# Performance work log

Hardware: AMD Instinct MI355X
Metric: run time of the kernel (lower is better)

Reference implementation:

```python
import jax, jax.numpy as jnp
import numpy as np

N = 100000
E = 1600000
IN_C, HID_C, OUT_C = 128, 64, 16


def setup_inputs() -> dict:
    key = jax.random.key(0)
    k1, k2, k3, k4, k5 = jax.random.split(key, 5)
    x = jax.random.normal(k1, (N, IN_C), dtype=jnp.float32)
    edge_index = jax.random.randint(k2, (2, E), 0, N, dtype=jnp.int64)
    edge_weight = jax.random.uniform(k3, (E,), dtype=jnp.float32)
    # GCNConv weights (Glorot init, bias=False)
    W1 = jax.random.normal(k4, (IN_C, HID_C), dtype=jnp.float32) * (1.0 / np.sqrt(IN_C))
    W2 = jax.random.normal(k5, (HID_C, OUT_C), dtype=jnp.float32) * (1.0 / np.sqrt(HID_C))
    return {"x": x, "edge_index": edge_index, "edge_weight": edge_weight, "W1": W1, "W2": W2}


def _gcn_norm(edge_index, edge_weight, num_nodes):
    # add self loops with weight 1 (PyG gcn_norm with add_self_loops=True)
    loop = jnp.arange(num_nodes, dtype=edge_index.dtype)
    row = jnp.concatenate([edge_index[0], loop])
    col = jnpp_concat = jnp.concatenate([edge_index[1], loop])
    w = jnp.concatenate([edge_weight, jnp.ones((num_nodes,), edge_weight.dtype)])
    deg = jax.ops.segment_sum(w, col, num_segments=num_nodes)
    dinv = jnp.where(deg > 0, jax.lax.rsqrt(deg), 0.0)
    norm = dinv[row] * w * dinv[col]
    return row, col, norm


def _gcn_conv(x, W, row, col, norm, num_nodes):
    h = x @ W                              # [N, C_out] dense projection
    msg = h[row] * norm[:, None]           # gather + scale per edge
    return jax.ops.segment_sum(msg, col, num_segments=num_nodes)  # scatter-add at dst


def reference(x, edge_index, edge_weight, W1, W2):
    num_nodes = x.shape[0]
    row, col, norm = _gcn_norm(edge_index, edge_weight, num_nodes)
    h = _gcn_conv(x, W1, row, col, norm, num_nodes)
    h = jax.nn.relu(h)  # dropout_rate == 0 / eval -> identity
    h = _gcn_conv(h, W2, row, col, norm, num_nodes)
    return jax.nn.log_softmax(h, axis=1)
```

## Files before the change

### kernel.cpp

```cpp
#include <hip/hip_runtime.h>
#include <hip/hip_fp16.h>
#include <math.h>

constexpr int IN_C = 128, HID_C = 64, OUT_C = 16;
constexpr int BSH = 7;
constexpr int BCAP = 2560;
constexpr int REC_PT = BCAP / 256;
constexpr int TILE = 4096;
constexpr float WSC = 33554432.0f;
constexpr float WINV15 = 1.0f / 32768.0f;

using f16x8 = __attribute__((ext_vector_type(8))) _Float16;
using f16x4 = __attribute__((ext_vector_type(4))) _Float16;
using f32x4 = __attribute__((ext_vector_type(4))) float;

__global__ __launch_bounds__(256) void k_tile(const int* __restrict__ row, const int* __restrict__ col,
                                              const float* __restrict__ w, int* __restrict__ histG,
                                              uint2* __restrict__ rec, int E, int nb) {
  __shared__ int hcnt[1024];
  __shared__ int hoff[1024];
  __shared__ int cs[256];
  int t = threadIdx.x, tile = blockIdx.x;
  for (int i = t; i < 1024; i += 256) hcnt[i] = 0;
  __syncthreads();
  int base = tile * TILE;
#pragma unroll
  for (int u = 0; u < TILE / 256; ++u) {
    int e = base + u * 256 + t;
    if (e < E) atomicAdd(&hcnt[col[e] >> BSH], 1);
  }
  __syncthreads();
  int c0 = hcnt[4 * t] + hcnt[4 * t + 1] + hcnt[4 * t + 2] + hcnt[4 * t + 3];
  cs[t] = c0;
  __syncthreads();
  for (int off = 1; off < 256; off <<= 1) {
    int v = (t >= off) ? cs[t - off] : 0;
    __syncthreads();
    cs[t] += v;
    __syncthreads();
  }
  int r0 = cs[t] - c0;
  hoff[4 * t] = r0; r0 += hcnt[4 * t];
  hoff[4 * t + 1] = r0; r0 += hcnt[4 * t + 1];
  hoff[4 * t + 2] = r0; r0 += hcnt[4 * t + 2];
  hoff[4 * t + 3] = r0;
  __syncthreads();
  for (int i = t; i < nb; i += 256)
    histG[(size_t)tile * nb + i] = (hoff[i] << 13) | hcnt[i];
  __syncthreads();
#pragma unroll
  for (int u = 0; u < TILE / 256; ++u) {
    int e = base + u * 256 + t;
    if (e < E) {
      int r = row[e], d = col[e];
      int b = d >> BSH;
      unsigned lo = (unsigned)(d & ((1 << BSH) - 1));
      unsigned wf = __float2uint_rn(w[e] * WSC);
      if (wf > 33554431u) wf = 33554431u;
      int slot = atomicAdd(&hoff[b], 1);
      rec[(size_t)tile * TILE + slot] = make_uint2((unsigned)r, (lo << 25) | wf);
    }
  }
}

__global__ __launch_bounds__(256) void k_buck2(const int* __restrict__ histG, const uint2* __restrict__ rec,
                                               unsigned* __restrict__ pairs, int* __restrict__ ptrg,
                                               int* __restrict__ cntg, float* __restrict__ dinvg,
                                               int n, int T, int nb) {
  int b = blockIdx.x, t = threadIdx.x;
  __shared__ int s[512];
  __shared__ int off_s[512];
  __shared__ int lcnt[128];
  __shared__ float lws[128];
  __shared__ int lptr[128];
  __shared__ unsigned sp[BCAP];
  int i0 = t, i1 = t + 256;
  int v0 = (i0 < T) ? histG[(size_t)i0 * nb + b] : 0;
  int v1 = (i1 < T) ? histG[(size_t)i1 * nb + b] : 0;
  off_s[i0] = v0 >> 13; off_s[i1] = v1 >> 13;
  s[i0] = v0 & 8191; s[i1] = v1 & 8191;
  if (t < 128) { lcnt[t] = 0; lws[t] = 0.f; }
  __syncthreads();
  for (int off = 1; off < 512; off <<= 1) {
    int a0 = (i0 >= off) ? s[i0 - off] : 0;
    int a1 = (i1 >= off) ? s[i1 - off] : 0;
    __syncthreads();
    s[i0] += a0; s[i1] += a1;
    __syncthreads();
  }
  int cnt = s[511];
  if (cnt > BCAP) cnt = BCAP;
  uint2 rv[REC_PT];
  int rk[REC_PT];
#pragma unroll
  for (int u = 0; u < REC_PT; ++u) {
    int i = u * 256 + t;
    if (i < cnt) {
      int lo_ = 0, hi_ = 511;
      while (lo_ < hi_) { int m = (lo_ + hi_) >> 1; if (s[m] > i) hi_ = m; else lo_ = m + 1; }
      int seg = lo_;
      int ex = seg ? s[seg - 1] : 0;
      uint2 v = rec[(size_t)seg * TILE + off_s[seg] + (i - ex)];
      rv[u] = v;
      int lo = v.y >> 25;
      rk[u] = atomicAdd(&lcnt[lo], 1);
      atomicAdd(&lws[lo], (float)(v.y & 0x1FFFFFFu) * (1.0f / WSC));
    }
  }
  __syncthreads();
  if (t < 128) lptr[t] = lcnt[t];
  __syncthreads();
  for (int off = 1; off < 128; off <<= 1) {
    int v = (t < 128 && t >= off) ? lptr[t - off] : 0;
    __syncthreads();
    if (t < 128 && t >= off) lptr[t] += v;
    __syncthreads();
  }
  if (t < 128) {
    int d = (b << BSH) + t;
    if (d < n) {
      ptrg[d] = b * BCAP + lptr[t] - lcnt[t];
      cntg[d] = lcnt[t];
      dinvg[d] = rsqrtf(1.0f + lws[t]);
    }
  }
#pragma unroll
  for (int u = 0; u < REC_PT; ++u) {
    int i = u * 256 + t;
    if (i < cnt) {
      uint2 v = rv[u];
      int lo = v.y >> 25;
      unsigned wq = ((v.y & 0x1FFFFFFu) + 512u) >> 10;
      if (wq > 32767u) wq = 32767u;
      sp[(lptr[lo] - lcnt[lo]) + rk[u]] = (v.x << 15) | wq;
    }
  }
  __syncthreads();
  for (int i = t; i < cnt; i += 256)
    pairs[(size_t)b * BCAP + i] = sp[i];
}

__global__ __launch_bounds__(256) void k_gemm1(const float* __restrict__ x, const float* __restrict__ W1,
                                               const float* __restrict__ dinv,
                                               __half* __restrict__ h1h, int n) {
  __shared__ _Float16 w1t[HID_C][IN_C];
  int t = threadIdx.x;
  for (int i = t; i < IN_C * HID_C / 4; i += 256) {
    float4 v = ((const float4*)W1)[i];
    int k = (i * 4) / HID_C;
    int c = (i * 4) % HID_C;
    w1t[c + 0][k] = (_Float16)v.x;
    w1t[c + 1][k] = (_Float16)v.y;
    w1t[c + 2][k] = (_Float16)v.z;
    w1t[c + 3][k] = (_Float16)v.w;
  }
  __syncthreads();
  int wave = t >> 6, lane = t & 63;
  int row0 = (blockIdx.x * 4 + wave) * 16;
  if (row0 >= n) return;
  int lrow = lane & 15, lkg = lane >> 4;
  bool rvalid = (row0 + lrow) < n;
  const float* xr = x + (size_t)(row0 + lrow) * IN_C;
  f32x4 acc[4];
#pragma unroll
  for (int cg = 0; cg < 4; ++cg) acc[cg] = (f32x4){0.f, 0.f, 0.f, 0.f};
#pragma unroll
  for (int ks = 0; ks < 4; ++ks) {
    int k0 = ks * 32 + lkg * 8;
    f16x8 a;
    if (rvalid) {
      float4 u0 = *(const float4*)&xr[k0];
      float4 u1 = *(const float4*)&xr[k0 + 4];
      a[0] = (_Float16)u0.x; a[1] = (_Float16)u0.y; a[2] = (_Float16)u0.z; a[3] = (_Float16)u0.w;
      a[4] = (_Float16)u1.x; a[5] = (_Float16)u1.y; a[6] = (_Float16)u1.z; a[7] = (_Float16)u1.w;
    } else {
#pragma unroll
      for (int j = 0; j < 8; ++j) a[j] = (_Float16)0.f;
    }
#pragma unroll
    for (int cg = 0; cg < 4; ++cg) {
      f16x8 bfrag = *(const f16x8*)&w1t[cg * 16 + lrow][k0];
      acc[cg] = __builtin_amdgcn_mfma_f32_16x16x32_f16(a, bfrag, acc[cg], 0, 0, 0);
    }
  }
  float dv[4];
#pragma unroll
  for (int r = 0; r < 4; ++r) {
    int gr = row0 + lkg * 4 + r;
    dv[r] = (gr < n) ? dinv[gr] : 0.f;
  }
#pragma unroll
  for (int cg = 0; cg < 4; ++cg) {
#pragma unroll
    for (int r = 0; r < 4; ++r) {
      int gr = row0 + lkg * 4 + r;
      if (gr < n)
        h1h[(size_t)gr * HID_C + cg * 16 + lrow] = __float2half_rn(dv[r] * acc[cg][r]);
    }
  }
}

__global__ __launch_bounds__(256) void k_agg1f(const int* __restrict__ ptr, const int* __restrict__ cnt,
                                               const unsigned* __restrict__ pairs, const float* __restrict__ dinv,
                                               const __half* __restrict__ h1h, const float* __restrict__ W2,
                                               __half* __restrict__ h2h, int n) {
  __shared__ float w2s[HID_C * OUT_C];
  __shared__ __align__(16) float s[4][68];
  int t = threadIdx.x;
  ((float4*)w2s)[t] = ((const float4*)W2)[t];
  __syncthreads();
  int wv = t >> 6, lane = t & 63;
  int g = lane >> 4;
  int c4 = (lane & 15) * 4;
  int d = blockIdx.x * 4 + wv;
  if (d < n) {
    d = __builtin_amdgcn_readfirstlane(d);
    int k = ptr[d], end = k + cnt[d];
    float dd = dinv[d];
    f32x4 acc = {0.f, 0.f, 0.f, 0.f};
    if (g == 0) {
      f16x4 sv = *(const f16x4*)&h1h[(size_t)d * HID_C + c4];
      acc[0] = (float)sv[0]; acc[1] = (float)sv[1];
      acc[2] = (float)sv[2]; acc[3] = (float)sv[3];
    }
    int last = end - 1;
    for (; k < end; k += 32) {
      unsigned p[8]; float w[8]; f16x4 v[8];
#pragma unroll
      for (int u = 0; u < 8; ++u) {
        int idx = k + u * 4 + g;
        int ic = (idx <= last) ? idx : last;
        p[u] = pairs[ic];
        w[u] = (idx <= last) ? (float)(p[u] & 32767u) * WINV15 : 0.f;
      }
#pragma unroll
      for (int u = 0; u < 8; ++u)
        v[u] = *(const f16x4*)&h1h[(size_t)(p[u] >> 15) * HID_C + c4];
#pragma unroll
      for (int u = 0; u < 8; ++u) {
        acc[0] = fmaf(w[u], (float)v[u][0], acc[0]);
        acc[1] = fmaf(w[u], (float)v[u][1], acc[1]);
        acc[2] = fmaf(w[u], (float)v[u][2], acc[2]);
        acc[3] = fmaf(w[u], (float)v[u][3], acc[3]);
      }
    }
#pragma unroll
    for (int i = 0; i < 4; ++i) {
      acc[i] += __shfl_xor(acc[i], 16);
      acc[i] += __shfl_xor(acc[i], 32);
    }
    if (g == 0) {
      float4 r;
      r.x = fmaxf(dd * acc[0], 0.f);
      r.y = fmaxf(dd * acc[1], 0.f);
      r.z = fmaxf(dd * acc[2], 0.f);
      r.w = fmaxf(dd * acc[3], 0.f);
      *(float4*)&s[wv][c4] = r;
    }
  } else {
    if (g == 0) *(float4*)&s[wv][c4] = make_float4(0.f, 0.f, 0.f, 0.f);
  }
  __syncthreads();
  if (t < 64) {
    int nl = t >> 4, j = t & 15;
    int dn = blockIdx.x * 4 + nl;
    if (dn < n) {
      float a2 = 0.f;
#pragma unroll
      for (int c = 0; c < HID_C; ++c) a2 = fmaf(s[nl][c], w2s[c * OUT_C + j], a2);
      h2h[(size_t)dn * OUT_C + j] = __float2half_rn(dinv[dn] * a2);
    }
  }
}

__global__ __launch_bounds__(256) void k_agg2(const int* __restrict__ ptr, const int* __restrict__ cnt,
                                              const unsigned* __restrict__ pairs, const float* __restrict__ dinv,
                                              const __half* __restrict__ h2h, float* __restrict__ out, int n) {
  int t = threadIdx.x;
  int d = blockIdx.x * 16 + (t >> 4);
  if (d >= n) return;
  int j = t & 15;
  int k = ptr[d], end = k + cnt[d];
  float dd = dinv[d];
  float acc = __half2float(h2h[(size_t)d * OUT_C + j]);
  for (; k + 8 <= end; k += 8) {
    unsigned p[8];
    float v[8];
#pragma unroll
    for (int u = 0; u < 8; ++u) p[u] = pairs[k + u];
#pragma unroll
    for (int u = 0; u < 8; ++u)
      v[u] = __half2float(h2h[(size_t)(p[u] >> 15) * OUT_C + j]);
#pragma unroll
    for (int u = 0; u < 8; ++u) acc = fmaf((float)(p[u] & 32767u) * WINV15, v[u], acc);
  }
  if (k + 4 <= end) {
    unsigned p[4];
    float v[4];
#pragma unroll
    for (int u = 0; u < 4; ++u) p[u] = pairs[k + u];
#pragma unroll
    for (int u = 0; u < 4; ++u)
      v[u] = __half2float(h2h[(size_t)(p[u] >> 15) * OUT_C + j]);
#pragma unroll
    for (int u = 0; u < 4; ++u) acc = fmaf((float)(p[u] & 32767u) * WINV15, v[u], acc);
    k += 4;
  }
  for (; k < end; ++k) {
    unsigned p = pairs[k];
    acc = fmaf((float)(p & 32767u) * WINV15, __half2float(h2h[(size_t)(p >> 15) * OUT_C + j]), acc);
  }
  float lg = dd * acc;
  float mx = lg;
#pragma unroll
  for (int off = 8; off; off >>= 1) mx = fmaxf(mx, __shfl_xor(mx, off, 16));
  float sm = expf(lg - mx);
#pragma unroll
  for (int off = 8; off; off >>= 1) sm += __shfl_xor(sm, off, 16);
  out[(size_t)d * OUT_C + j] = lg - mx - logf(sm);
}

extern "C" void kernel_launch(void* const* d_in, const int* in_sizes, int n_in,
                              void* d_out, int out_size, void* d_ws, size_t ws_size,
                              hipStream_t stream) {
  const float* x  = (const float*)d_in[0];
  const int*   ei = (const int*)d_in[1];
  const float* ew = (const float*)d_in[2];
  const float* W1 = (const float*)d_in[3];
  const float* W2 = (const float*)d_in[4];
  const int N = in_sizes[0] / IN_C;
  const int E = in_sizes[2];
  const int* row = ei;
  const int* col = ei + E;
  float* out = (float*)d_out;
  const int NBUK = (N + (1 << BSH) - 1) >> BSH;
  const int T = (E + TILE - 1) / TILE;

  char* p = (char*)d_ws;
  unsigned* pairs = (unsigned*)p;     p += (size_t)NBUK * BCAP * 4;
  int*   ptr  = (int*)p;              p += (size_t)N * 4;
  int*   cnt  = (int*)p;              p += (size_t)N * 4;
  float* dinv = (float*)p;            p += (size_t)N * 4;
  int*   histG= (int*)p;              p += (size_t)T * NBUK * 4;
  char*  uni  = p;                    p += (size_t)N * HID_C * 4;
  uint2* rec  = (uint2*)uni;
  __half* h1h = (__half*)uni;
  __half* h2h = (__half*)(uni + (size_t)N * HID_C * 2);

  dim3 b(256);
  k_tile <<<T, b, 0, stream>>>(row, col, ew, histG, rec, E, NBUK);
  k_buck2<<<NBUK, b, 0, stream>>>(histG, rec, pairs, ptr, cnt, dinv, N, T, NBUK);
  k_gemm1<<<(N + 63) / 64, b, 0, stream>>>(x, W1, dinv, h1h, N);
  k_agg1f<<<(N + 3) / 4, b, 0, stream>>>(ptr, cnt, pairs, dinv, h1h, W2, h2h, N);
  k_agg2 <<<(N + 15) / 16, b, 0, stream>>>(ptr, cnt, pairs, dinv, h2h, out, N);
}
```

Baseline: 142.7 us.

## Fuse edge tiling with GEMM1 and fold source normalization into edge weights

Merges the edge-bucketing kernel and the first dense projection into one launch using block-index partitioning and a shared-memory union, so the two independent stages overlap. To make GEMM1 independent of dinv, degree sums are accumulated by global atomics into a memset wsum buffer. The source-side dinv factor is folded into the quantized per-edge weights in the bucketing kernel, while the destination-side factor is applied in the aggregation kernels. In exchange it adds 1.6M global float atomics, an extra memset, and per-edge random reads of wsum, and rec no longer aliases h1h, which raises workspace use.

```diff
diff --git a/kernel.cpp b/kernel.cpp
--- a/kernel.cpp
+++ b/kernel.cpp
@@ -14,56 +14,115 @@
 using f16x4 = __attribute__((ext_vector_type(4))) _Float16;
 using f32x4 = __attribute__((ext_vector_type(4))) float;
 
-__global__ __launch_bounds__(256) void k_tile(const int* __restrict__ row, const int* __restrict__ col,
-                                              const float* __restrict__ w, int* __restrict__ histG,
-                                              uint2* __restrict__ rec, int E, int nb) {
-  __shared__ int hcnt[1024];
-  __shared__ int hoff[1024];
-  __shared__ int cs[256];
-  int t = threadIdx.x, tile = blockIdx.x;
-  for (int i = t; i < 1024; i += 256) hcnt[i] = 0;
-  __syncthreads();
-  int base = tile * TILE;
-#pragma unroll
-  for (int u = 0; u < TILE / 256; ++u) {
-    int e = base + u * 256 + t;
-    if (e < E) atomicAdd(&hcnt[col[e] >> BSH], 1);
-  }
-  __syncthreads();
-  int c0 = hcnt[4 * t] + hcnt[4 * t + 1] + hcnt[4 * t + 2] + hcnt[4 * t + 3];
-  cs[t] = c0;
-  __syncthreads();
-  for (int off = 1; off < 256; off <<= 1) {
-    int v = (t >= off) ? cs[t - off] : 0;
-    __syncthreads();
-    cs[t] += v;
-    __syncthreads();
-  }
-  int r0 = cs[t] - c0;
-  hoff[4 * t] = r0; r0 += hcnt[4 * t];
-  hoff[4 * t + 1] = r0; r0 += hcnt[4 * t + 1];
-  hoff[4 * t + 2] = r0; r0 += hcnt[4 * t + 2];
-  hoff[4 * t + 3] = r0;
-  __syncthreads();
-  for (int i = t; i < nb; i += 256)
-    histG[(size_t)tile * nb + i] = (hoff[i] << 13) | hcnt[i];
-  __syncthreads();
-#pragma unroll
-  for (int u = 0; u < TILE / 256; ++u) {
-    int e = base + u * 256 + t;
-    if (e < E) {
-      int r = row[e], d = col[e];
-      int b = d >> BSH;
-      unsigned lo = (unsigned)(d & ((1 << BSH) - 1));
-      unsigned wf = __float2uint_rn(w[e] * WSC);
-      if (wf > 33554431u) wf = 33554431u;
-      int slot = atomicAdd(&hoff[b], 1);
-      rec[(size_t)tile * TILE + slot] = make_uint2((unsigned)r, (lo << 25) | wf);
+__global__ __launch_bounds__(256) void k_fused(const float* __restrict__ x, const float* __restrict__ W1,
+                                               const int* __restrict__ row, const int* __restrict__ col,
+                                               const float* __restrict__ w, int* __restrict__ histG,
+                                               uint2* __restrict__ rec, float* __restrict__ wsum,
+                                               __half* __restrict__ h1h, int E, int n, int nb, int T) {
+  __shared__ union SM {
+    struct { int hcnt[1024]; int hoff[1024]; int cs[256]; } t;
+    _Float16 w1t[HID_C][IN_C];
+  } sm;
+  int t = threadIdx.x;
+  if ((int)blockIdx.x < T) {
+    int tile = blockIdx.x;
+    for (int i = t; i < 1024; i += 256) sm.t.hcnt[i] = 0;
+    __syncthreads();
+    int base = tile * TILE;
+    int colv[TILE / 256];
+#pragma unroll
+    for (int u = 0; u < TILE / 256; ++u) {
+      int e = base + u * 256 + t;
+      colv[u] = (e < E) ? col[e] : -1;
+      if (e < E) atomicAdd(&sm.t.hcnt[colv[u] >> BSH], 1);
+    }
+    __syncthreads();
+    int c0 = sm.t.hcnt[4 * t] + sm.t.hcnt[4 * t + 1] + sm.t.hcnt[4 * t + 2] + sm.t.hcnt[4 * t + 3];
+    sm.t.cs[t] = c0;
+    __syncthreads();
+    for (int off = 1; off < 256; off <<= 1) {
+      int v = (t >= off) ? sm.t.cs[t - off] : 0;
+      __syncthreads();
+      sm.t.cs[t] += v;
+      __syncthreads();
+    }
+    int r0 = sm.t.cs[t] - c0;
+    sm.t.hoff[4 * t] = r0; r0 += sm.t.hcnt[4 * t];
+    sm.t.hoff[4 * t + 1] = r0; r0 += sm.t.hcnt[4 * t + 1];
+    sm.t.hoff[4 * t + 2] = r0; r0 += sm.t.hcnt[4 * t + 2];
+    sm.t.hoff[4 * t + 3] = r0;
+    __syncthreads();
+    for (int i = t; i < nb; i += 256)
+      histG[(size_t)tile * nb + i] = (sm.t.hoff[i] << 13) | sm.t.hcnt[i];
+    __syncthreads();
+#pragma unroll
+    for (int u = 0; u < TILE / 256; ++u) {
+      int e = base + u * 256 + t;
+      if (e < E) {
+        int r = row[e], d = colv[u];
+        int b = d >> BSH;
+        unsigned lo = (unsigned)(d & ((1 << BSH) - 1));
+        float wv = w[e];
+        atomicAdd(&wsum[d], wv);
+        unsigned wf = __float2uint_rn(wv * WSC);
+        if (wf > 33554431u) wf = 33554431u;
+        int slot = atomicAdd(&sm.t.hoff[b], 1);
+        rec[(size_t)tile * TILE + slot] = make_uint2((unsigned)r, (lo << 25) | wf);
+      }
+    }
+    return;
+  }
+  for (int i = t; i < IN_C * HID_C / 4; i += 256) {
+    float4 v = ((const float4*)W1)[i];
+    int k = (i * 4) / HID_C;
+    int c = (i * 4) % HID_C;
+    sm.w1t[c + 0][k] = (_Float16)v.x;
+    sm.w1t[c + 1][k] = (_Float16)v.y;
+    sm.w1t[c + 2][k] = (_Float16)v.z;
+    sm.w1t[c + 3][k] = (_Float16)v.w;
+  }
+  __syncthreads();
+  int wave = t >> 6, lane = t & 63;
+  int row0 = (((int)blockIdx.x - T) * 4 + wave) * 16;
+  if (row0 >= n) return;
+  int lrow = lane & 15, lkg = lane >> 4;
+  bool rvalid = (row0 + lrow) < n;
+  const float* xr = x + (size_t)(row0 + lrow) * IN_C;
+  f32x4 acc[4];
+#pragma unroll
+  for (int cg = 0; cg < 4; ++cg) acc[cg] = (f32x4){0.f, 0.f, 0.f, 0.f};
+#pragma unroll
+  for (int ks = 0; ks < 4; ++ks) {
+    int k0 = ks * 32 + lkg * 8;
+    f16x8 a;
+    if (rvalid) {
+      float4 u0 = *(const float4*)&xr[k0];
+      float4 u1 = *(const float4*)&xr[k0 + 4];
+      a[0] = (_Float16)u0.x; a[1] = (_Float16)u0.y; a[2] = (_Float16)u0.z; a[3] = (_Float16)u0.w;
+      a[4] = (_Float16)u1.x; a[5] = (_Float16)u1.y; a[6] = (_Float16)u1.z; a[7] = (_Float16)u1.w;
+    } else {
+#pragma unroll
+      for (int j = 0; j < 8; ++j) a[j] = (_Float16)0.f;
+    }
+#pragma unroll
+    for (int cg = 0; cg < 4; ++cg) {
+      f16x8 bfrag = *(const f16x8*)&sm.w1t[cg * 16 + lrow][k0];
+      acc[cg] = __builtin_amdgcn_mfma_f32_16x16x32_f16(a, bfrag, acc[cg], 0, 0, 0);
+    }
+  }
+#pragma unroll
+  for (int cg = 0; cg < 4; ++cg) {
+#pragma unroll
+    for (int r = 0; r < 4; ++r) {
+      int gr = row0 + lkg * 4 + r;
+      if (gr < n)
+        h1h[(size_t)gr * HID_C + cg * 16 + lrow] = __float2half_rn(acc[cg][r]);
     }
   }
 }
 
 __global__ __launch_bounds__(256) void k_buck2(const int* __restrict__ histG, const uint2* __restrict__ rec,
+                                               const float* __restrict__ wsum,
                                                unsigned* __restrict__ pairs, int* __restrict__ ptrg,
                                                int* __restrict__ cntg, float* __restrict__ dinvg,
                                                int n, int T, int nb) {
@@ -71,7 +130,6 @@
   __shared__ int s[512];
   __shared__ int off_s[512];
   __shared__ int lcnt[128];
-  __shared__ float lws[128];
   __shared__ int lptr[128];
   __shared__ unsigned sp[BCAP];
   int i0 = t, i1 = t + 256;
@@ -79,7 +137,7 @@
   int v1 = (i1 < T) ? histG[(size_t)i1 * nb + b] : 0;
   off_s[i0] = v0 >> 13; off_s[i1] = v1 >> 13;
   s[i0] = v0 & 8191; s[i1] = v1 & 8191;
-  if (t < 128) { lcnt[t] = 0; lws[t] = 0.f; }
+  if (t < 128) lcnt[t] = 0;
   __syncthreads();
   for (int off = 1; off < 512; off <<= 1) {
     int a0 = (i0 >= off) ? s[i0 - off] : 0;
@@ -102,9 +160,7 @@
       int ex = seg ? s[seg - 1] : 0;
       uint2 v = rec[(size_t)seg * TILE + off_s[seg] + (i - ex)];
       rv[u] = v;
-      int lo = v.y >> 25;
-      rk[u] = atomicAdd(&lcnt[lo], 1);
-      atomicAdd(&lws[lo], (float)(v.y & 0x1FFFFFFu) * (1.0f / WSC));
+      rk[u] = atomicAdd(&lcnt[v.y >> 25], 1);
     }
   }
   __syncthreads();
@@ -121,7 +177,7 @@
     if (d < n) {
       ptrg[d] = b * BCAP + lptr[t] - lcnt[t];
       cntg[d] = lcnt[t];
-      dinvg[d] = rsqrtf(1.0f + lws[t]);
+      dinvg[d] = rsqrtf(1.0f + wsum[d]);
     }
   }
 #pragma unroll
@@ -130,7 +186,9 @@
     if (i < cnt) {
       uint2 v = rv[u];
       int lo = v.y >> 25;
-      unsigned wq = ((v.y & 0x1FFFFFFu) + 512u) >> 10;
+      float dsrc = rsqrtf(1.0f + wsum[v.x]);
+      float wv = (float)(v.y & 0x1FFFFFFu) * (1.0f / WSC) * dsrc;
+      unsigned wq = __float2uint_rn(wv * 32768.0f);
       if (wq > 32767u) wq = 32767u;
       sp[(lptr[lo] - lcnt[lo]) + rk[u]] = (v.x << 15) | wq;
     }
@@ -138,66 +196,6 @@
   __syncthreads();
   for (int i = t; i < cnt; i += 256)
     pairs[(size_t)b * BCAP + i] = sp[i];
-}
-
-__global__ __launch_bounds__(256) void k_gemm1(const float* __restrict__ x, const float* __restrict__ W1,
-                                               const float* __restrict__ dinv,
-                                               __half* __restrict__ h1h, int n) {
-  __shared__ _Float16 w1t[HID_C][IN_C];
-  int t = threadIdx.x;
-  for (int i = t; i < IN_C * HID_C / 4; i += 256) {
-    float4 v = ((const float4*)W1)[i];
-    int k = (i * 4) / HID_C;
-    int c = (i * 4) % HID_C;
-    w1t[c + 0][k] = (_Float16)v.x;
-    w1t[c + 1][k] = (_Float16)v.y;
-    w1t[c + 2][k] = (_Float16)v.z;
-    w1t[c + 3][k] = (_Float16)v.w;
-  }
-  __syncthreads();
-  int wave = t >> 6, lane = t & 63;
-  int row0 = (blockIdx.x * 4 + wave) * 16;
-  if (row0 >= n) return;
-  int lrow = lane & 15, lkg = lane >> 4;
-  bool rvalid = (row0 + lrow) < n;
-  const float* xr = x + (size_t)(row0 + lrow) * IN_C;
-  f32x4 acc[4];
-#pragma unroll
-  for (int cg = 0; cg < 4; ++cg) acc[cg] = (f32x4){0.f, 0.f, 0.f, 0.f};
-#pragma unroll
-  for (int ks = 0; ks < 4; ++ks) {
-    int k0 = ks * 32 + lkg * 8;
-    f16x8 a;
-    if (rvalid) {
-      float4 u0 = *(const float4*)&xr[k0];
-      float4 u1 = *(const float4*)&xr[k0 + 4];
-      a[0] = (_Float16)u0.x; a[1] = (_Float16)u0.y; a[2] = (_Float16)u0.z; a[3] = (_Float16)u0.w;
-      a[4] = (_Float16)u1.x; a[5] = (_Float16)u1.y; a[6] = (_Float16)u1.z; a[7] = (_Float16)u1.w;
-    } else {
-#pragma unroll
-      for (int j = 0; j < 8; ++j) a[j] = (_Float16)0.f;
-    }
-#pragma unroll
-    for (int cg = 0; cg < 4; ++cg) {
-      f16x8 bfrag = *(const f16x8*)&w1t[cg * 16 + lrow][k0];
-      acc[cg] = __builtin_amdgcn_mfma_f32_16x16x32_f16(a, bfrag, acc[cg], 0, 0, 0);
-    }
-  }
-  float dv[4];
-#pragma unroll
-  for (int r = 0; r < 4; ++r) {
-    int gr = row0 + lkg * 4 + r;
-    dv[r] = (gr < n) ? dinv[gr] : 0.f;
-  }
-#pragma unroll
-  for (int cg = 0; cg < 4; ++cg) {
-#pragma unroll
-    for (int r = 0; r < 4; ++r) {
-      int gr = row0 + lkg * 4 + r;
-      if (gr < n)
-        h1h[(size_t)gr * HID_C + cg * 16 + lrow] = __float2half_rn(dv[r] * acc[cg][r]);
-    }
-  }
 }
 
 __global__ __launch_bounds__(256) void k_agg1f(const int* __restrict__ ptr, const int* __restrict__ cnt,
@@ -220,8 +218,8 @@
     f32x4 acc = {0.f, 0.f, 0.f, 0.f};
     if (g == 0) {
       f16x4 sv = *(const f16x4*)&h1h[(size_t)d * HID_C + c4];
-      acc[0] = (float)sv[0]; acc[1] = (float)sv[1];
-      acc[2] = (float)sv[2]; acc[3] = (float)sv[3];
+      acc[0] = dd * (float)sv[0]; acc[1] = dd * (float)sv[1];
+      acc[2] = dd * (float)sv[2]; acc[3] = dd * (float)sv[3];
     }
     int last = end - 1;
     for (; k < end; k += 32) {
@@ -268,7 +266,7 @@
       float a2 = 0.f;
 #pragma unroll
       for (int c = 0; c < HID_C; ++c) a2 = fmaf(s[nl][c], w2s[c * OUT_C + j], a2);
-      h2h[(size_t)dn * OUT_C + j] = __float2half_rn(dinv[dn] * a2);
+      h2h[(size_t)dn * OUT_C + j] = __float2half_rn(a2);
     }
   }
 }
@@ -282,7 +280,7 @@
   int j = t & 15;
   int k = ptr[d], end = k + cnt[d];
   float dd = dinv[d];
-  float acc = __half2float(h2h[(size_t)d * OUT_C + j]);
+  float acc = dd * __half2float(h2h[(size_t)d * OUT_C + j]);
   for (; k + 8 <= end; k += 8) {
     unsigned p[8];
     float v[8];
@@ -335,22 +333,23 @@
   float* out = (float*)d_out;
   const int NBUK = (N + (1 << BSH) - 1) >> BSH;
   const int T = (E + TILE - 1) / TILE;
+  const int G = (N + 63) / 64;
 
   char* p = (char*)d_ws;
   unsigned* pairs = (unsigned*)p;     p += (size_t)NBUK * BCAP * 4;
   int*   ptr  = (int*)p;              p += (size_t)N * 4;
   int*   cnt  = (int*)p;              p += (size_t)N * 4;
   float* dinv = (float*)p;            p += (size_t)N * 4;
+  float* wsum = (float*)p;            p += (size_t)N * 4;
   int*   histG= (int*)p;              p += (size_t)T * NBUK * 4;
-  char*  uni  = p;                    p += (size_t)N * HID_C * 4;
-  uint2* rec  = (uint2*)uni;
-  __half* h1h = (__half*)uni;
-  __half* h2h = (__half*)(uni + (size_t)N * HID_C * 2);
+  uint2* rec  = (uint2*)p;            p += (size_t)T * TILE * 8;
+  __half* h1h = (__half*)p;           p += (size_t)N * HID_C * 2;
+  __half* h2h = (__half*)p;           p += (size_t)N * OUT_C * 2;
 
   dim3 b(256);
-  k_tile <<<T, b, 0, stream>>>(row, col, ew, histG, rec, E, NBUK);
-  k_buck2<<<NBUK, b, 0, stream>>>(histG, rec, pairs, ptr, cnt, dinv, N, T, NBUK);
-  k_gemm1<<<(N + 63) / 64, b, 0, stream>>>(x, W1, dinv, h1h, N);
+  hipMemsetAsync(wsum, 0, (size_t)N * 4, stream);
+  k_fused<<<T + G, b, 0, stream>>>(x, W1, row, col, ew, histG, rec, wsum, h1h, E, N, NBUK, T);
+  k_buck2<<<NBUK, b, 0, stream>>>(histG, rec, wsum, pairs, ptr, cnt, dinv, N, T, NBUK);
   k_agg1f<<<(N + 3) / 4, b, 0, stream>>>(ptr, cnt, pairs, dinv, h1h, W2, h2h, N);
   k_agg2 <<<(N + 15) / 16, b, 0, stream>>>(ptr, cnt, pairs, dinv, h2h, out, N);
 }
```

After: 209.4 us. 46.7% more time.
